# Kernel optimization log

Measured on AMD Instinct MI355X. Metric: run time of the kernel, lower is better.

## Reference

```python
import jax, jax.numpy as jnp
import numpy as np

N = 30000      # nodes
E = 480000     # edges (before self-loops)
IN = 32        # input_dim
H = 8          # heads
C = 64         # hidden_dim (per-head out channels)
HC = H * C     # 512, concat width
L = 3          # num_layers
NEG_SLOPE = 0.2  # PyG GATConv default


def setup_inputs() -> dict:
    key = jax.random.key(0)
    ks = jax.random.split(key, 16)
    s = 0.05
    return {
        "x": jax.random.normal(ks[0], (N, IN), jnp.float32),
        "edge_index": jax.random.randint(ks[1], (2, E), 0, N, jnp.int32),
        # input projection
        "W_in": jax.random.normal(ks[2], (IN, HC), jnp.float32) * s,
        "b_in": jnp.zeros((HC,), jnp.float32),
        # stacked GATConv params (L layers)
        "W_gat": jax.random.normal(ks[3], (L, HC, HC), jnp.float32) * s,
        "att_src": jax.random.normal(ks[4], (L, H, C), jnp.float32) * s,
        "att_dst": jax.random.normal(ks[5], (L, H, C), jnp.float32) * s,
        "b_gat": jnp.zeros((L, HC), jnp.float32),
        # heads
        "W_att": jax.random.normal(ks[6], (HC, H), jnp.float32) * s,
        "b_att": jnp.zeros((H,), jnp.float32),
        "W_h1": jax.random.normal(ks[7], (HC, C), jnp.float32) * s,
        "b_h1": jnp.zeros((C,), jnp.float32),
        "W_h2": jax.random.normal(ks[8], (C, 1), jnp.float32) * s,
        "b_h2": jnp.zeros((1,), jnp.float32),
    }


def _gat_layer(h, src, dst, W, a_src, a_dst, b):
    # h: [N, HC]; src/dst: [E'] (with self-loops)
    hp = (h @ W).reshape(N, H, C)                       # per-head features
    s = jnp.einsum('nhc,hc->nh', hp, a_src)             # [N, H]
    d = jnp.einsum('nhc,hc->nh', hp, a_dst)             # [N, H]
    e = jax.nn.leaky_relu(s[src] + d[dst], NEG_SLOPE)   # [E', H]
    # segment softmax over destination neighborhoods
    m = jax.ops.segment_max(e, dst, num_segments=N)     # [N, H]
    ex = jnp.exp(e - m[dst])
    den = jax.ops.segment_sum(ex, dst, num_segments=N)
    alpha = ex / (den[dst] + 1e-16)                     # [E', H]
    msg = hp[src] * alpha[:, :, None]                   # [E', H, C]
    out = jax.ops.segment_sum(msg, dst, num_segments=N).reshape(N, HC) + b
    return out


def reference(x, edge_index, W_in, b_in, W_gat, att_src, att_dst, b_gat,
              W_att, b_att, W_h1, b_h1, W_h2, b_h2):
    # PyG GATConv adds self-loops by default
    loops = jnp.arange(N, dtype=edge_index.dtype)
    src = jnp.concatenate([edge_index[0], loops])
    dst = jnp.concatenate([edge_index[1], loops])

    h = jax.nn.relu(x @ W_in + b_in)                    # input_proj + ReLU
    for l in range(L):
        h = jax.nn.relu(_gat_layer(h, src, dst, W_gat[l], att_src[l], att_dst[l], b_gat[l]))
        # dropout is identity in eval mode
    attention_weights = jax.nn.softmax(h @ W_att + b_att, axis=1)   # [N, H]
    anomaly_scores = jax.nn.sigmoid(jax.nn.relu(h @ W_h1 + b_h1) @ W_h2 + b_h2)  # [N, 1]
    return (anomaly_scores, attention_weights)
```

## Files before the change

kernel.cpp:

```cpp
#include <hip/hip_runtime.h>
#include <hip/hip_bf16.h>
#include <math.h>

#define HCW 512
#define NHD 8
#define CCH 64

typedef unsigned short u16;
typedef unsigned int   u32;
typedef __attribute__((ext_vector_type(8))) short bf16x8;
typedef __attribute__((ext_vector_type(4))) float f32x4;

__device__ __forceinline__ float bf2f(u32 u) {
  union { float f; u32 i; } v; v.i = u << 16; return v.f;
}
__device__ __forceinline__ u16 f2bf(float f) {
  u32 x = __builtin_bit_cast(u32, f);
  return (u16)((x + 0x7fff + ((x >> 16) & 1)) >> 16);
}
__device__ __forceinline__ void gload_lds16(const void* g, void* l) {
  __builtin_amdgcn_global_load_lds(
      (const __attribute__((address_space(1))) u32*)g,
      (__attribute__((address_space(3))) u32*)l, 16, 0, 0);
}

__global__ void k_hist(const int* __restrict__ ei, int* __restrict__ deg, int E, int N) {
  int e = blockIdx.x * blockDim.x + threadIdx.x;
  if (e >= E + N) return;
  int dst = (e < E) ? ei[E + e] : (e - E);
  atomicAdd(&deg[dst], 1);
}

__global__ __launch_bounds__(256) void k_alloc(const int* __restrict__ deg, int* __restrict__ beg,
                                               int* __restrict__ cursor, int N) {
  int n = blockIdx.x * 256 + threadIdx.x;
  int lane = threadIdx.x & 63;
  int v = (n < N) ? deg[n] : 0;
  int incl = v;
  #pragma unroll
  for (int off = 1; off < 64; off <<= 1) {
    int t = __shfl_up(incl, off);
    if (lane >= off) incl += t;
  }
  int total = __shfl(incl, 63);
  int base = 0;
  if (lane == 63) base = atomicAdd(cursor, total);
  base = __shfl(base, 63);
  if (n < N) beg[n] = base + incl - v;
}

__global__ void k_fill(const int* __restrict__ ei, const int* __restrict__ beg,
                       int* __restrict__ cnt, int* __restrict__ csr_src, int E, int N) {
  int e = blockIdx.x * blockDim.x + threadIdx.x;
  if (e >= E + N) return;
  int src, dst;
  if (e < E) { src = ei[e]; dst = ei[E + e]; } else { src = e - E; dst = e - E; }
  int pos = beg[dst] + atomicAdd(&cnt[dst], 1);
  csr_src[pos] = src;
}

__global__ __launch_bounds__(256) void k_prep(const float* __restrict__ W_gat, u16* __restrict__ Wt,
                                              const float* __restrict__ W_h1, const float* __restrict__ W_att,
                                              u16* __restrict__ Wf,
                                              const float* __restrict__ x, u16* __restrict__ xb, int xtotal,
                                              const float* __restrict__ W_in, u16* __restrict__ Wtin,
                                              int XB) {
  __shared__ float sm[32][33];
  int b = blockIdx.x;
  int t = threadIdx.x;
  if (b < 768) {
    int l = b >> 8, rem = b & 255;
    int n0 = (rem & 15) * 32, k0 = (rem >> 4) * 32;
    const float* Wl = W_gat + (size_t)l * HCW * HCW;
    u16* Wtl = Wt + (size_t)l * HCW * HCW;
    int tx = t & 31, ty = t >> 5;
    #pragma unroll
    for (int r = 0; r < 32; r += 8)
      sm[ty + r][tx] = Wl[(size_t)(k0 + ty + r) * HCW + n0 + tx];
    __syncthreads();
    #pragma unroll
    for (int r = 0; r < 32; r += 8)
      Wtl[(size_t)(n0 + ty + r) * HCW + k0 + tx] = f2bf(sm[tx][ty + r]);
  } else if (b < 848) {
    int n = b - 768;
    for (int k = t; k < 512; k += 256) {
      float v = 0.f;
      if (n < 64) v = W_h1[(size_t)k * 64 + n];
      else if (n < 72) v = W_att[(size_t)k * 8 + (n - 64)];
      Wf[(size_t)n * 512 + k] = f2bf(v);
    }
  } else if (b < 848 + XB) {
    int i = ((b - 848) * 256 + t) * 8;
    if (i < xtotal) {
      float4 a = *(const float4*)(x + i);
      float4 bb = *(const float4*)(x + i + 4);
      uint4 o;
      o.x = (u32)f2bf(a.x) | ((u32)f2bf(a.y) << 16);
      o.y = (u32)f2bf(a.z) | ((u32)f2bf(a.w) << 16);
      o.z = (u32)f2bf(bb.x) | ((u32)f2bf(bb.y) << 16);
      o.w = (u32)f2bf(bb.z) | ((u32)f2bf(bb.w) << 16);
      *(uint4*)(xb + i) = o;
    }
  } else {
    int idx = (b - 848 - XB) * 256 + t;
    int n = idx >> 5, k = idx & 31;
    Wtin[idx] = f2bf(W_in[(size_t)k * HCW + n]);
  }
}

__global__ __launch_bounds__(256) void k_inproj3(const u16* __restrict__ xb, const u16* __restrict__ Wt,
                                                 const float* __restrict__ b, u16* __restrict__ h, int N) {
  __shared__ u16 As[128 * 32];
  __shared__ u16 Bs[128 * 32];
  int tid = threadIdx.x, lane = tid & 63, w = tid >> 6;
  int bm = blockIdx.y * 128, bn = blockIdx.x * 128;
  #pragma unroll
  for (int it = 0; it < 4; it++) {
    int g = it * 256 + tid;
    if (g < 512) {
      int row = g >> 2, gb = g & 3, gs = gb ^ (row & 3);
      int ar = bm + row; if (ar >= N) ar = N - 1;
      gload_lds16(xb + (size_t)ar * 32 + gs * 8, &As[g * 8]);
    } else {
      int gg = g - 512;
      int row = gg >> 2, gb = gg & 3, gs = gb ^ (row & 3);
      gload_lds16(Wt + (size_t)(bn + row) * 32 + gs * 8, &Bs[gg * 8]);
    }
  }
  __syncthreads();
  bf16x8 af[2];
  #pragma unroll
  for (int i = 0; i < 2; i++) {
    int rowA = w * 32 + i * 16 + (lane & 15);
    int gA = (lane >> 4) ^ (rowA & 3);
    af[i] = *(const bf16x8*)&As[rowA * 32 + gA * 8];
  }
  f32x4 acc[2][8] = {};
  #pragma unroll
  for (int j = 0; j < 8; j++) {
    int rowB = j * 16 + (lane & 15);
    int gB = (lane >> 4) ^ (rowB & 3);
    bf16x8 bfr = *(const bf16x8*)&Bs[rowB * 32 + gB * 8];
    #pragma unroll
    for (int i = 0; i < 2; i++)
      acc[i][j] = __builtin_amdgcn_mfma_f32_16x16x32_bf16(af[i], bfr, acc[i][j], 0, 0, 0);
  }
  #pragma unroll
  for (int j = 0; j < 8; j++) {
    int col = bn + j * 16 + (lane & 15);
    float bb = b[col];
    #pragma unroll
    for (int i = 0; i < 2; i++) {
      #pragma unroll
      for (int r = 0; r < 4; r++) {
        int n = bm + w * 32 + i * 16 + (lane >> 4) * 4 + r;
        if (n < N) h[(size_t)n * HCW + col] = f2bf(fmaxf(acc[i][j][r] + bb, 0.f));
      }
    }
  }
}

__global__ __launch_bounds__(256) void k_gemm_mfma(const u16* __restrict__ A,
                                                   const u16* __restrict__ Bt,
                                                   u16* __restrict__ C,
                                                   const float* __restrict__ a_src,
                                                   const float* __restrict__ a_dst,
                                                   float* __restrict__ sarr,
                                                   float* __restrict__ darr,
                                                   int M) {
  int nPanels = (M + 127) >> 7;
  int lin = blockIdx.y * 4 + blockIdx.x;
  int xcd = lin & 7;
  int t = lin >> 3;
  int bn_i = t & 3;
  int p = t >> 2;
  int bm_i = p * 8 + xcd;
  if (bm_i >= nPanels) return;
  int bm = bm_i * 128, bn = bn_i * 128;

  __shared__ u16 As[128 * 64];
  __shared__ u16 Bs[128 * 64];
  int tid = threadIdx.x;
  int lane = tid & 63, w = tid >> 6;
  int wr = w >> 1, wc = w & 1;
  f32x4 acc[4][4] = {};
  for (int k0 = 0; k0 < 512; k0 += 64) {
    __syncthreads();
    #pragma unroll
    for (int it = 0; it < 4; it++) {
      int g = it * 256 + tid;
      int row = g >> 3;
      int gb = g & 7;
      int gs = gb ^ (row & 7);
      int ar = bm + row; if (ar >= M) ar = M - 1;
      gload_lds16(A + (size_t)ar * HCW + k0 + gs * 8, &As[g * 8]);
      gload_lds16(Bt + (size_t)(bn + row) * HCW + k0 + gs * 8, &Bs[g * 8]);
    }
    __syncthreads();
    #pragma unroll
    for (int ks = 0; ks < 2; ks++) {
      bf16x8 af[4], bfr[4];
      #pragma unroll
      for (int f = 0; f < 4; f++) {
        int rowA = wr * 64 + f * 16 + (lane & 15);
        int gA = ((ks * 4 + (lane >> 4)) ^ (rowA & 7));
        af[f] = *(const bf16x8*)&As[rowA * 64 + gA * 8];
        int rowB = wc * 64 + f * 16 + (lane & 15);
        int gB = ((ks * 4 + (lane >> 4)) ^ (rowB & 7));
        bfr[f] = *(const bf16x8*)&Bs[rowB * 64 + gB * 8];
      }
      #pragma unroll
      for (int i = 0; i < 4; i++)
        #pragma unroll
        for (int j = 0; j < 4; j++)
          acc[i][j] = __builtin_amdgcn_mfma_f32_16x16x32_bf16(af[i], bfr[j], acc[i][j], 0, 0, 0);
    }
  }
  int gr_base = bm + wr * 64;
  int gc_base = bn + wc * 64;
  #pragma unroll
  for (int i = 0; i < 4; i++) {
    #pragma unroll
    for (int j = 0; j < 4; j++) {
      int col = gc_base + j * 16 + (lane & 15);
      #pragma unroll
      for (int r = 0; r < 4; r++) {
        int rowg = gr_base + i * 16 + (lane >> 4) * 4 + r;
        if (rowg < M) C[(size_t)rowg * HCW + col] = f2bf(acc[i][j][r]);
      }
    }
  }
  int head = (bn >> 6) + wc;
  float asv[4], adv[4];
  #pragma unroll
  for (int j = 0; j < 4; j++) {
    asv[j] = a_src[head * 64 + j * 16 + (lane & 15)];
    adv[j] = a_dst[head * 64 + j * 16 + (lane & 15)];
  }
  #pragma unroll
  for (int i = 0; i < 4; i++) {
    #pragma unroll
    for (int r = 0; r < 4; r++) {
      float sv = acc[i][0][r] * asv[0] + acc[i][1][r] * asv[1]
               + acc[i][2][r] * asv[2] + acc[i][3][r] * asv[3];
      float dv = acc[i][0][r] * adv[0] + acc[i][1][r] * adv[1]
               + acc[i][2][r] * adv[2] + acc[i][3][r] * adv[3];
      sv += __shfl_xor(sv, 1); dv += __shfl_xor(dv, 1);
      sv += __shfl_xor(sv, 2); dv += __shfl_xor(dv, 2);
      sv += __shfl_xor(sv, 4); dv += __shfl_xor(dv, 4);
      sv += __shfl_xor(sv, 8); dv += __shfl_xor(dv, 8);
      if ((lane & 15) == 0) {
        int rowg = gr_base + i * 16 + (lane >> 4) * 4 + r;
        if (rowg < M) {
          sarr[(size_t)rowg * NHD + head] = sv;
          darr[(size_t)rowg * NHD + head] = dv;
        }
      }
    }
  }
}

__global__ __launch_bounds__(256) void k_agg7(const int* __restrict__ beg_, const int* __restrict__ deg_,
                                              const int* __restrict__ csr_src,
                                              const u16* __restrict__ hp, const float* __restrict__ s,
                                              const float* __restrict__ d, const float* __restrict__ bias,
                                              u16* __restrict__ hout, int N) {
  int wv = threadIdx.x >> 6, lane = threadIdx.x & 63;
  int n = blockIdx.x * 4 + wv;
  if (n >= N) return;
  int hd = lane >> 3;
  int c = lane * 8;
  int beg = beg_[n], end = beg + deg_[n];
  float dn = d[(size_t)n * NHD + hd];
  float acc[8] = {0.f, 0.f, 0.f, 0.f, 0.f, 0.f, 0.f, 0.f};
  float den = 0.f;

  int i = beg;
  for (; i + 8 <= end; i += 8) {
    int sidx[8];
    #pragma unroll
    for (int u = 0; u < 8; u++) sidx[u] = csr_src[i + u];
    float ev[8];
    #pragma unroll
    for (int u = 0; u < 8; u++) ev[u] = s[(size_t)sidx[u] * NHD + hd] + dn;
    uint4 v[8];
    #pragma unroll
    for (int u = 0; u < 8; u++) v[u] = *(const uint4*)(hp + (size_t)sidx[u] * HCW + c);
    #pragma unroll
    for (int u = 0; u < 8; u++) {
      float e = ev[u];
      e = (e > 0.f) ? e : 0.2f * e;
      float a = __expf(e);
      den += a;
      u32 w0 = v[u].x, w1 = v[u].y, w2 = v[u].z, w3 = v[u].w;
      acc[0] += a * bf2f(w0 & 0xffff); acc[1] += a * bf2f(w0 >> 16);
      acc[2] += a * bf2f(w1 & 0xffff); acc[3] += a * bf2f(w1 >> 16);
      acc[4] += a * bf2f(w2 & 0xffff); acc[5] += a * bf2f(w2 >> 16);
      acc[6] += a * bf2f(w3 & 0xffff); acc[7] += a * bf2f(w3 >> 16);
    }
  }
  for (; i < end; i++) {
    int s0 = csr_src[i];
    float e = s[(size_t)s0 * NHD + hd] + dn;
    uint4 v0 = *(const uint4*)(hp + (size_t)s0 * HCW + c);
    e = (e > 0.f) ? e : 0.2f * e;
    float a = __expf(e);
    den += a;
    u32 w0 = v0.x, w1 = v0.y, w2 = v0.z, w3 = v0.w;
    acc[0] += a * bf2f(w0 & 0xffff); acc[1] += a * bf2f(w0 >> 16);
    acc[2] += a * bf2f(w1 & 0xffff); acc[3] += a * bf2f(w1 >> 16);
    acc[4] += a * bf2f(w2 & 0xffff); acc[5] += a * bf2f(w2 >> 16);
    acc[6] += a * bf2f(w3 & 0xffff); acc[7] += a * bf2f(w3 >> 16);
  }

  float inv = 1.f / (den + 1e-16f);
  float4 bv0 = *(const float4*)(bias + c);
  float4 bv1 = *(const float4*)(bias + c + 4);
  float bb[8] = {bv0.x, bv0.y, bv0.z, bv0.w, bv1.x, bv1.y, bv1.z, bv1.w};
  u32 out[4];
  #pragma unroll
  for (int j = 0; j < 4; j++) {
    float o0 = fmaxf(acc[2 * j] * inv + bb[2 * j], 0.f);
    float o1 = fmaxf(acc[2 * j + 1] * inv + bb[2 * j + 1], 0.f);
    out[j] = (u32)f2bf(o0) | ((u32)f2bf(o1) << 16);
  }
  *(uint4*)(hout + (size_t)n * HCW + c) = make_uint4(out[0], out[1], out[2], out[3]);
}

__global__ __launch_bounds__(256) void k_final2(const u16* __restrict__ A,
                                                const u16* __restrict__ Wf,
                                                const float* __restrict__ b_att,
                                                const float* __restrict__ b_h1,
                                                const float* __restrict__ W_h2,
                                                const float* __restrict__ b_h2,
                                                float* __restrict__ anomaly, float* __restrict__ attw,
                                                int M) {
  __shared__ u16 As[128 * 64];
  __shared__ u16 Bs[80 * 64];
  __shared__ float so[4][32][84];
  int tid = threadIdx.x;
  int lane = tid & 63, w = tid >> 6;
  int bm = blockIdx.x * 128;
  f32x4 acc[2][5] = {};
  for (int k0 = 0; k0 < 512; k0 += 64) {
    __syncthreads();
    #pragma unroll
    for (int it = 0; it < 7; it++) {
      int g = it * 256 + tid;
      if (g < 1024) {
        int row = g >> 3, gb = g & 7;
        int gs = gb ^ (row & 7);
        int ar = bm + row; if (ar >= M) ar = M - 1;
        gload_lds16(A + (size_t)ar * HCW + k0 + gs * 8, &As[g * 8]);
      } else if (g < 1664) {
        int gg = g - 1024;
        int row = gg >> 3, gb = gg & 7;
        int gs = gb ^ (row & 7);
        gload_lds16(Wf + (size_t)row * 512 + k0 + gs * 8, &Bs[gg * 8]);
      }
    }
    __syncthreads();
    #pragma unroll
    for (int ks = 0; ks < 2; ks++) {
      bf16x8 af[2], bfr[5];
      #pragma unroll
      for (int i = 0; i < 2; i++) {
        int rowA = w * 32 + i * 16 + (lane & 15);
        int gA = ((ks * 4 + (lane >> 4)) ^ (rowA & 7));
        af[i] = *(const bf16x8*)&As[rowA * 64 + gA * 8];
      }
      #pragma unroll
      for (int j = 0; j < 5; j++) {
        int rowB = j * 16 + (lane & 15);
        int gB = ((ks * 4 + (lane >> 4)) ^ (rowB & 7));
        bfr[j] = *(const bf16x8*)&Bs[rowB * 64 + gB * 8];
      }
      #pragma unroll
      for (int i = 0; i < 2; i++)
        #pragma unroll
        for (int j = 0; j < 5; j++)
          acc[i][j] = __builtin_amdgcn_mfma_f32_16x16x32_bf16(af[i], bfr[j], acc[i][j], 0, 0, 0);
    }
  }
  #pragma unroll
  for (int i = 0; i < 2; i++) {
    #pragma unroll
    for (int j = 0; j < 5; j++) {
      int col = j * 16 + (lane & 15);
      #pragma unroll
      for (int r = 0; r < 4; r++) {
        int row_l = i * 16 + (lane >> 4) * 4 + r;
        so[w][row_l][col] = acc[i][j][r];
      }
    }
  }
  int row_l = lane >> 1, half = lane & 1;
  int n = bm + w * 32 + row_l;
  if (n < M) {
    float hacc = 0.f;
    #pragma unroll
    for (int kk = 0; kk < 32; kk++) {
      int cc = half * 32 + kk;
      float v = fmaxf(so[w][row_l][cc] + b_h1[cc], 0.f);
      hacc += v * W_h2[cc];
    }
    hacc += __shfl_xor(hacc, 1);
    if (half == 0) {
      anomaly[n] = 1.f / (1.f + __expf(-(hacc + b_h2[0])));
    } else {
      float lg[8];
      float mx = -1e30f;
      #pragma unroll
      for (int j = 0; j < 8; j++) {
        lg[j] = so[w][row_l][64 + j] + b_att[j];
        mx = fmaxf(mx, lg[j]);
      }
      float sum = 0.f;
      #pragma unroll
      for (int j = 0; j < 8; j++) { lg[j] = __expf(lg[j] - mx); sum += lg[j]; }
      float inv = 1.f / sum;
      #pragma unroll
      for (int j = 0; j < 8; j++) attw[(size_t)n * 8 + j] = lg[j] * inv;
    }
  }
}

extern "C" void kernel_launch(void* const* d_in, const int* in_sizes, int n_in,
                              void* d_out, int out_size, void* d_ws, size_t ws_size,
                              hipStream_t stream) {
  const float* x       = (const float*)d_in[0];
  const int*   ei      = (const int*)d_in[1];
  const float* W_in    = (const float*)d_in[2];
  const float* b_in    = (const float*)d_in[3];
  const float* W_gat   = (const float*)d_in[4];
  const float* att_src = (const float*)d_in[5];
  const float* att_dst = (const float*)d_in[6];
  const float* b_gat   = (const float*)d_in[7];
  const float* W_att   = (const float*)d_in[8];
  const float* b_att   = (const float*)d_in[9];
  const float* W_h1    = (const float*)d_in[10];
  const float* b_h1    = (const float*)d_in[11];
  const float* W_h2    = (const float*)d_in[12];
  const float* b_h2    = (const float*)d_in[13];

  const int N  = in_sizes[0] / 32;
  const int E  = in_sizes[1] / 2;
  const int ET = E + N;

  char* ws = (char*)d_ws;
  size_t off = 0;
  auto alloc = [&](size_t bytes) -> void* {
    void* p = ws + off;
    off = (off + bytes + 255) & ~(size_t)255;
    return p;
  };
  u16* h     = (u16*)alloc((size_t)N * HCW * 2);
  u16* hp    = (u16*)alloc((size_t)N * HCW * 2);
  u16* Wt    = (u16*)alloc((size_t)3 * HCW * HCW * 2);
  u16* Wf    = (u16*)alloc((size_t)80 * 512 * 2);
  u16* xb    = (u16*)alloc((size_t)N * 32 * 2);
  u16* Wtin  = (u16*)alloc((size_t)512 * 32 * 2);
  float* sarr = (float*)alloc((size_t)N * NHD * 4);
  float* darr = (float*)alloc((size_t)N * NHD * 4);
  int* zbuf   = (int*)alloc((size_t)(2 * N + 64) * 4);
  int* deg    = zbuf;
  int* cnt    = zbuf + N;
  int* cursor = zbuf + 2 * N;
  int* beg    = (int*)alloc((size_t)N * 4);
  int* csr    = (int*)alloc((size_t)ET * 4);

  float* anomaly = (float*)d_out;
  float* attw    = (float*)d_out + N;

  hipMemsetAsync(zbuf, 0, (size_t)(2 * N + 1) * 4, stream);

  int gbE = (ET + 255) / 256;
  int nb  = (N + 255) / 256;
  k_hist<<<gbE, 256, 0, stream>>>(ei, deg, E, N);
  k_alloc<<<nb, 256, 0, stream>>>(deg, beg, cursor, N);
  k_fill<<<gbE, 256, 0, stream>>>(ei, beg, cnt, csr, E, N);

  int xtotal = N * 32;
  int XB = (xtotal / 8 + 255) / 256;
  k_prep<<<848 + XB + 64, 256, 0, stream>>>(W_gat, Wt, W_h1, W_att, Wf, x, xb, xtotal,
                                            W_in, Wtin, XB);
  k_inproj3<<<dim3(4, (N + 127) / 128), 256, 0, stream>>>(xb, Wtin, b_in, h, N);

  int nPanels = (N + 127) / 128;
  int nPanelsPad = ((nPanels + 7) / 8) * 8;
  dim3 ggrid(4, nPanelsPad);
  for (int l = 0; l < 3; l++) {
    k_gemm_mfma<<<ggrid, 256, 0, stream>>>(h, Wt + (size_t)l * HCW * HCW, hp,
                                           att_src + (size_t)l * NHD * CCH,
                                           att_dst + (size_t)l * NHD * CCH,
                                           sarr, darr, N);
    k_agg7<<<(N + 3) / 4, 256, 0, stream>>>(beg, deg, csr, hp, sarr, darr,
                                            b_gat + (size_t)l * HCW, h, N);
  }

  k_final2<<<(N + 127) / 128, 256, 0, stream>>>(h, Wf, b_att, b_h1, W_h2, b_h2,
                                                anomaly, attw, N);
}
```

Before: 431.1 us.

## Split GAT aggregation across heads with per-head blocks and edge-parallel half-waves

```diff
diff --git a/kernel.cpp b/kernel.cpp
--- a/kernel.cpp
+++ b/kernel.cpp
@@ -260,71 +260,65 @@
   }
 }
 
-__global__ __launch_bounds__(256) void k_agg7(const int* __restrict__ beg_, const int* __restrict__ deg_,
+__global__ __launch_bounds__(256) void k_agg8(const int* __restrict__ beg_, const int* __restrict__ deg_,
                                               const int* __restrict__ csr_src,
                                               const u16* __restrict__ hp, const float* __restrict__ s,
                                               const float* __restrict__ d, const float* __restrict__ bias,
                                               u16* __restrict__ hout, int N) {
+  int hd = blockIdx.x;
   int wv = threadIdx.x >> 6, lane = threadIdx.x & 63;
-  int n = blockIdx.x * 4 + wv;
+  int half = lane >> 5;
+  int c = hd * 64 + (lane & 31) * 2;
+  int n = blockIdx.y * 4 + wv;
   if (n >= N) return;
-  int hd = lane >> 3;
-  int c = lane * 8;
-  int beg = beg_[n], end = beg + deg_[n];
+  int beg = beg_[n], dg = deg_[n];
+  int end = beg + dg;
   float dn = d[(size_t)n * NHD + hd];
-  float acc[8] = {0.f, 0.f, 0.f, 0.f, 0.f, 0.f, 0.f, 0.f};
-  float den = 0.f;
-
-  int i = beg;
-  for (; i + 8 <= end; i += 8) {
-    int sidx[8];
-    #pragma unroll
-    for (int u = 0; u < 8; u++) sidx[u] = csr_src[i + u];
-    float ev[8];
-    #pragma unroll
-    for (int u = 0; u < 8; u++) ev[u] = s[(size_t)sidx[u] * NHD + hd] + dn;
-    uint4 v[8];
-    #pragma unroll
-    for (int u = 0; u < 8; u++) v[u] = *(const uint4*)(hp + (size_t)sidx[u] * HCW + c);
-    #pragma unroll
-    for (int u = 0; u < 8; u++) {
-      float e = ev[u];
-      e = (e > 0.f) ? e : 0.2f * e;
-      float a = __expf(e);
-      den += a;
-      u32 w0 = v[u].x, w1 = v[u].y, w2 = v[u].z, w3 = v[u].w;
-      acc[0] += a * bf2f(w0 & 0xffff); acc[1] += a * bf2f(w0 >> 16);
-      acc[2] += a * bf2f(w1 & 0xffff); acc[3] += a * bf2f(w1 >> 16);
-      acc[4] += a * bf2f(w2 & 0xffff); acc[5] += a * bf2f(w2 >> 16);
-      acc[6] += a * bf2f(w3 & 0xffff); acc[7] += a * bf2f(w3 >> 16);
-    }
-  }
-  for (; i < end; i++) {
+  float a0 = 0.f, a1 = 0.f, den = 0.f;
+
+  int i = beg + half;
+  for (; i + 6 < end; i += 8) {
+    int s0 = csr_src[i], s1 = csr_src[i + 2], s2 = csr_src[i + 4], s3 = csr_src[i + 6];
+    float e0 = s[(size_t)s0 * NHD + hd] + dn;
+    float e1 = s[(size_t)s1 * NHD + hd] + dn;
+    float e2 = s[(size_t)s2 * NHD + hd] + dn;
+    float e3 = s[(size_t)s3 * NHD + hd] + dn;
+    u32 p0 = *(const u32*)(hp + (size_t)s0 * HCW + c);
+    u32 p1 = *(const u32*)(hp + (size_t)s1 * HCW + c);
+    u32 p2 = *(const u32*)(hp + (size_t)s2 * HCW + c);
+    u32 p3 = *(const u32*)(hp + (size_t)s3 * HCW + c);
+    e0 = (e0 > 0.f) ? e0 : 0.2f * e0;
+    e1 = (e1 > 0.f) ? e1 : 0.2f * e1;
+    e2 = (e2 > 0.f) ? e2 : 0.2f * e2;
+    e3 = (e3 > 0.f) ? e3 : 0.2f * e3;
+    float x0 = __expf(e0), x1 = __expf(e1), x2 = __expf(e2), x3 = __expf(e3);
+    den += (x0 + x1) + (x2 + x3);
+    a0 += x0 * bf2f(p0 & 0xffff) + x1 * bf2f(p1 & 0xffff)
+        + x2 * bf2f(p2 & 0xffff) + x3 * bf2f(p3 & 0xffff);
+    a1 += x0 * bf2f(p0 >> 16) + x1 * bf2f(p1 >> 16)
+        + x2 * bf2f(p2 >> 16) + x3 * bf2f(p3 >> 16);
+  }
+  for (; i < end; i += 2) {
     int s0 = csr_src[i];
-    float e = s[(size_t)s0 * NHD + hd] + dn;
-    uint4 v0 = *(const uint4*)(hp + (size_t)s0 * HCW + c);
-    e = (e > 0.f) ? e : 0.2f * e;
-    float a = __expf(e);
-    den += a;
-    u32 w0 = v0.x, w1 = v0.y, w2 = v0.z, w3 = v0.w;
-    acc[0] += a * bf2f(w0 & 0xffff); acc[1] += a * bf2f(w0 >> 16);
-    acc[2] += a * bf2f(w1 & 0xffff); acc[3] += a * bf2f(w1 >> 16);
-    acc[4] += a * bf2f(w2 & 0xffff); acc[5] += a * bf2f(w2 >> 16);
-    acc[6] += a * bf2f(w3 & 0xffff); acc[7] += a * bf2f(w3 >> 16);
-  }
-
+    float e0 = s[(size_t)s0 * NHD + hd] + dn;
+    u32 p0 = *(const u32*)(hp + (size_t)s0 * HCW + c);
+    e0 = (e0 > 0.f) ? e0 : 0.2f * e0;
+    float x0 = __expf(e0);
+    den += x0;
+    a0 += x0 * bf2f(p0 & 0xffff);
+    a1 += x0 * bf2f(p0 >> 16);
+  }
+
+  a0 += __shfl_xor(a0, 32);
+  a1 += __shfl_xor(a1, 32);
+  den += __shfl_xor(den, 32);
   float inv = 1.f / (den + 1e-16f);
-  float4 bv0 = *(const float4*)(bias + c);
-  float4 bv1 = *(const float4*)(bias + c + 4);
-  float bb[8] = {bv0.x, bv0.y, bv0.z, bv0.w, bv1.x, bv1.y, bv1.z, bv1.w};
-  u32 out[4];
-  #pragma unroll
-  for (int j = 0; j < 4; j++) {
-    float o0 = fmaxf(acc[2 * j] * inv + bb[2 * j], 0.f);
-    float o1 = fmaxf(acc[2 * j + 1] * inv + bb[2 * j + 1], 0.f);
-    out[j] = (u32)f2bf(o0) | ((u32)f2bf(o1) << 16);
-  }
-  *(uint4*)(hout + (size_t)n * HCW + c) = make_uint4(out[0], out[1], out[2], out[3]);
+  float o0 = fmaxf(a0 * inv + bias[c], 0.f);
+  float o1 = fmaxf(a1 * inv + bias[c + 1], 0.f);
+  if (half == 0) {
+    u32 packed = (u32)f2bf(o0) | ((u32)f2bf(o1) << 16);
+    *(u32*)(hout + (size_t)n * HCW + c) = packed;
+  }
 }
 
 __global__ __launch_bounds__(256) void k_final2(const u16* __restrict__ A,
@@ -489,13 +483,14 @@
   int nPanels = (N + 127) / 128;
   int nPanelsPad = ((nPanels + 7) / 8) * 8;
   dim3 ggrid(4, nPanelsPad);
+  dim3 agrid(8, (N + 3) / 4);
   for (int l = 0; l < 3; l++) {
     k_gemm_mfma<<<ggrid, 256, 0, stream>>>(h, Wt + (size_t)l * HCW * HCW, hp,
                                            att_src + (size_t)l * NHD * CCH,
                                            att_dst + (size_t)l * NHD * CCH,
                                            sarr, darr, N);
-    k_agg7<<<(N + 3) / 4, 256, 0, stream>>>(beg, deg, csr, hp, sarr, darr,
-                                            b_gat + (size_t)l * HCW, h, N);
+    k_agg8<<<agrid, 256, 0, stream>>>(beg, deg, csr, hp, sarr, darr,
+                                      b_gat + (size_t)l * HCW, h, N);
   }
 
   k_final2<<<(N + 127) / 128, 256, 0, stream>>>(h, Wf, b_att, b_h1, W_h2, b_h2,
```

Result: slower. 571.1 us (+32.5%).

## Split aggregation per head and parallelize edges across lane groups

Applied to the files above, without the earlier changes.

```diff
diff --git a/kernel.cpp b/kernel.cpp
--- a/kernel.cpp
+++ b/kernel.cpp
@@ -260,71 +260,78 @@
   }
 }
 
-__global__ __launch_bounds__(256) void k_agg7(const int* __restrict__ beg_, const int* __restrict__ deg_,
+__global__ __launch_bounds__(256) void k_agg9(const int* __restrict__ beg_, const int* __restrict__ deg_,
                                               const int* __restrict__ csr_src,
                                               const u16* __restrict__ hp, const float* __restrict__ s,
                                               const float* __restrict__ d, const float* __restrict__ bias,
                                               u16* __restrict__ hout, int N) {
+  int hd = blockIdx.x;
   int wv = threadIdx.x >> 6, lane = threadIdx.x & 63;
-  int n = blockIdx.x * 4 + wv;
+  int g = lane >> 3;
+  int q = lane & 7;
+  int c = hd * 64 + q * 8;
+  int n = blockIdx.y * 4 + wv;
   if (n >= N) return;
-  int hd = lane >> 3;
-  int c = lane * 8;
   int beg = beg_[n], end = beg + deg_[n];
   float dn = d[(size_t)n * NHD + hd];
   float acc[8] = {0.f, 0.f, 0.f, 0.f, 0.f, 0.f, 0.f, 0.f};
   float den = 0.f;
 
-  int i = beg;
-  for (; i + 8 <= end; i += 8) {
-    int sidx[8];
-    #pragma unroll
-    for (int u = 0; u < 8; u++) sidx[u] = csr_src[i + u];
-    float ev[8];
-    #pragma unroll
-    for (int u = 0; u < 8; u++) ev[u] = s[(size_t)sidx[u] * NHD + hd] + dn;
-    uint4 v[8];
-    #pragma unroll
-    for (int u = 0; u < 8; u++) v[u] = *(const uint4*)(hp + (size_t)sidx[u] * HCW + c);
-    #pragma unroll
-    for (int u = 0; u < 8; u++) {
-      float e = ev[u];
-      e = (e > 0.f) ? e : 0.2f * e;
-      float a = __expf(e);
-      den += a;
-      u32 w0 = v[u].x, w1 = v[u].y, w2 = v[u].z, w3 = v[u].w;
-      acc[0] += a * bf2f(w0 & 0xffff); acc[1] += a * bf2f(w0 >> 16);
-      acc[2] += a * bf2f(w1 & 0xffff); acc[3] += a * bf2f(w1 >> 16);
-      acc[4] += a * bf2f(w2 & 0xffff); acc[5] += a * bf2f(w2 >> 16);
-      acc[6] += a * bf2f(w3 & 0xffff); acc[7] += a * bf2f(w3 >> 16);
-    }
-  }
-  for (; i < end; i++) {
+  int i = beg + g;
+  for (; i + 8 < end; i += 16) {
+    int s0 = csr_src[i], s1 = csr_src[i + 8];
+    float e0 = s[(size_t)s0 * NHD + hd] + dn;
+    float e1 = s[(size_t)s1 * NHD + hd] + dn;
+    uint4 v0 = *(const uint4*)(hp + (size_t)s0 * HCW + c);
+    uint4 v1 = *(const uint4*)(hp + (size_t)s1 * HCW + c);
+    e0 = (e0 > 0.f) ? e0 : 0.2f * e0;
+    e1 = (e1 > 0.f) ? e1 : 0.2f * e1;
+    float x0 = __expf(e0), x1 = __expf(e1);
+    den += x0 + x1;
+    u32 w0[4] = {v0.x, v0.y, v0.z, v0.w};
+    u32 w1[4] = {v1.x, v1.y, v1.z, v1.w};
+    #pragma unroll
+    for (int j = 0; j < 4; j++) {
+      acc[2 * j]     += x0 * bf2f(w0[j] & 0xffff) + x1 * bf2f(w1[j] & 0xffff);
+      acc[2 * j + 1] += x0 * bf2f(w0[j] >> 16)    + x1 * bf2f(w1[j] >> 16);
+    }
+  }
+  for (; i < end; i += 8) {
     int s0 = csr_src[i];
-    float e = s[(size_t)s0 * NHD + hd] + dn;
+    float e0 = s[(size_t)s0 * NHD + hd] + dn;
     uint4 v0 = *(const uint4*)(hp + (size_t)s0 * HCW + c);
-    e = (e > 0.f) ? e : 0.2f * e;
-    float a = __expf(e);
-    den += a;
-    u32 w0 = v0.x, w1 = v0.y, w2 = v0.z, w3 = v0.w;
-    acc[0] += a * bf2f(w0 & 0xffff); acc[1] += a * bf2f(w0 >> 16);
-    acc[2] += a * bf2f(w1 & 0xffff); acc[3] += a * bf2f(w1 >> 16);
-    acc[4] += a * bf2f(w2 & 0xffff); acc[5] += a * bf2f(w2 >> 16);
-    acc[6] += a * bf2f(w3 & 0xffff); acc[7] += a * bf2f(w3 >> 16);
-  }
-
-  float inv = 1.f / (den + 1e-16f);
-  float4 bv0 = *(const float4*)(bias + c);
-  float4 bv1 = *(const float4*)(bias + c + 4);
-  float bb[8] = {bv0.x, bv0.y, bv0.z, bv0.w, bv1.x, bv1.y, bv1.z, bv1.w};
-  u32 out[4];
-  #pragma unroll
-  for (int j = 0; j < 4; j++) {
-    float o0 = fmaxf(acc[2 * j] * inv + bb[2 * j], 0.f);
-    float o1 = fmaxf(acc[2 * j + 1] * inv + bb[2 * j + 1], 0.f);
-    out[j] = (u32)f2bf(o0) | ((u32)f2bf(o1) << 16);
-  }
-  *(uint4*)(hout + (size_t)n * HCW + c) = make_uint4(out[0], out[1], out[2], out[3]);
+    e0 = (e0 > 0.f) ? e0 : 0.2f * e0;
+    float x0 = __expf(e0);
+    den += x0;
+    u32 w0[4] = {v0.x, v0.y, v0.z, v0.w};
+    #pragma unroll
+    for (int j = 0; j < 4; j++) {
+      acc[2 * j]     += x0 * bf2f(w0[j] & 0xffff);
+      acc[2 * j + 1] += x0 * bf2f(w0[j] >> 16);
+    }
+  }
+
+  #pragma unroll
+  for (int m = 8; m < 64; m <<= 1) {
+    den += __shfl_xor(den, m);
+    #pragma unroll
+    for (int j = 0; j < 8; j++) acc[j] += __shfl_xor(acc[j], m);
+  }
+
+  if (g == 0) {
+    float inv = 1.f / (den + 1e-16f);
+    float4 bv0 = *(const float4*)(bias + c);
+    float4 bv1 = *(const float4*)(bias + c + 4);
+    float bb[8] = {bv0.x, bv0.y, bv0.z, bv0.w, bv1.x, bv1.y, bv1.z, bv1.w};
+    u32 out[4];
+    #pragma unroll
+    for (int j = 0; j < 4; j++) {
+      float o0 = fmaxf(acc[2 * j] * inv + bb[2 * j], 0.f);
+      float o1 = fmaxf(acc[2 * j + 1] * inv + bb[2 * j + 1], 0.f);
+      out[j] = (u32)f2bf(o0) | ((u32)f2bf(o1) << 16);
+    }
+    *(uint4*)(hout + (size_t)n * HCW + c) = make_uint4(out[0], out[1], out[2], out[3]);
+  }
 }
 
 __global__ __launch_bounds__(256) void k_final2(const u16* __restrict__ A,
@@ -489,13 +496,14 @@
   int nPanels = (N + 127) / 128;
   int nPanelsPad = ((nPanels + 7) / 8) * 8;
   dim3 ggrid(4, nPanelsPad);
+  dim3 agrid(8, (N + 3) / 4);
   for (int l = 0; l < 3; l++) {
     k_gemm_mfma<<<ggrid, 256, 0, stream>>>(h, Wt + (size_t)l * HCW * HCW, hp,
                                            att_src + (size_t)l * NHD * CCH,
                                            att_dst + (size_t)l * NHD * CCH,
                                            sarr, darr, N);
-    k_agg7<<<(N + 3) / 4, 256, 0, stream>>>(beg, deg, csr, hp, sarr, darr,
-                                            b_gat + (size_t)l * HCW, h, N);
+    k_agg9<<<agrid, 256, 0, stream>>>(beg, deg, csr, hp, sarr, darr,
+                                      b_gat + (size_t)l * HCW, h, N);
   }
 
   k_final2<<<(N + 127) / 128, 256, 0, stream>>>(h, Wf, b_att, b_h1, W_h2, b_h2,
```

After: 497.6 us. 1.15x slower.
